# Kernel tuning notes

Hardware: AMD Instinct MI355X
Metric: run time of the kernel (lower is better)

Reference implementation:

```python
import jax, jax.numpy as jnp
import numpy as np

NUM_HEADS = 12
FEATURE_DIM = 16
HEAD_DIM = 128
EPS = 1e-12


def taylor_map(x):
    # x: [b, h, t, d] -> [b, h, t, 1 + d + d*d] (2nd-order Taylor features of exp)
    d = x.shape[-1]
    r2 = jnp.asarray(np.sqrt(2.0), x.dtype)
    rd = jnp.asarray(np.sqrt(d), x.dtype)
    rrd = jnp.asarray(np.sqrt(np.sqrt(d)), x.dtype)
    x2 = (x[..., :, None] * x[..., None, :]).reshape(x.shape[:-1] + (d * d,)) / r2
    ones = jnp.ones(x.shape[:-1] + (1,), x.dtype)
    return jnp.concatenate([ones, x / rrd, x2 / rd], axis=-1)


def setup_inputs() -> dict:
    key = jax.random.key(0)
    ks = jax.random.split(key, 5)
    b, t, hid = 2, 2048, 1536
    scale = 0.02
    return {
        "hidden_states": jax.random.normal(ks[0], (b, t, hid), jnp.float32),
        "Wq": jax.random.normal(ks[1], (NUM_HEADS * FEATURE_DIM, hid), jnp.float32) * scale,
        "Wk": jax.random.normal(ks[2], (NUM_HEADS * FEATURE_DIM, hid), jnp.float32) * scale,
        "Wv": jax.random.normal(ks[3], (NUM_HEADS * HEAD_DIM, hid), jnp.float32) * scale,
        "Wo": jax.random.normal(ks[4], (hid, NUM_HEADS * HEAD_DIM), jnp.float32) * scale,
    }


def reference(hidden_states, Wq, Wk, Wv, Wo):
    b, t, _ = hidden_states.shape
    H, dk, dv = NUM_HEADS, FEATURE_DIM, HEAD_DIM
    # projections (torch Linear: x @ W^T), split heads -> [b, h, t, d]
    q = (hidden_states @ Wq.T).reshape(b, t, H, dk).transpose(0, 2, 1, 3)
    k = (hidden_states @ Wk.T).reshape(b, t, H, dk).transpose(0, 2, 1, 3)
    v = (hidden_states @ Wv.T).reshape(b, t, H, dv).transpose(0, 2, 1, 3)
    qf = taylor_map(q)  # [b, h, t, D], D = 1 + dk + dk^2
    kf = taylor_map(k)
    # causal kernelized attention: identical math to cumsum-of-outer-products form
    S = jnp.einsum("bhtd,bhsd->bhts", qf, kf)  # [b, h, t, t]
    mask = jnp.tril(jnp.ones((t, t), bool))
    S = jnp.where(mask, S, jnp.zeros((), S.dtype))
    num = jnp.einsum("bhts,bhse->bhte", S, v)  # [b, h, t, dv]
    den = S.sum(-1) + EPS  # [b, h, t]
    y = num / den[..., None]
    y = y.transpose(0, 2, 1, 3).reshape(b, t, H * dv)
    return y @ Wo.T
```

## Files before the change

### kernel.cpp

```cpp
#include <hip/hip_runtime.h>

#define B 2
#define T 2048
#define HID 1536
#define NH 12
#define DK 16
#define DV 128
#define BT (B * T)
#define EPS 1e-12f

typedef __attribute__((ext_vector_type(8))) short bf16x8;
typedef __attribute__((ext_vector_type(4))) float f32x4;

__device__ __forceinline__ unsigned short f2bf(float f) {
    unsigned int u = __float_as_uint(f);
    u += 0x7FFFu + ((u >> 16) & 1u);
    return (unsigned short)(u >> 16);
}

__global__ __launch_bounds__(256) void cvt_all(const float* __restrict__ hs,
                                               const float* __restrict__ Wq,
                                               const float* __restrict__ Wk,
                                               const float* __restrict__ Wv,
                                               const float* __restrict__ Wo,
                                               unsigned short* __restrict__ hsb,
                                               unsigned short* __restrict__ wqk,
                                               unsigned short* __restrict__ wvb,
                                               unsigned short* __restrict__ wob) {
    int bx = blockIdx.x;
    const float* src;
    unsigned short* dst;
    if (bx < 3072)      { src = hs; dst = hsb; }
    else if (bx < 3216) { src = Wq; dst = wqk;          bx -= 3072; }
    else if (bx < 3360) { src = Wk; dst = wqk + 294912; bx -= 3216; }
    else if (bx < 4512) { src = Wv; dst = wvb;          bx -= 3360; }
    else                { src = Wo; dst = wob;          bx -= 4512; }
    const int i = (bx * 256 + threadIdx.x) * 8;
    float4 a = *(const float4*)(src + i);
    float4 b = *(const float4*)(src + i + 4);
    *(ushort4*)(dst + i)     = make_ushort4(f2bf(a.x), f2bf(a.y), f2bf(a.z), f2bf(a.w));
    *(ushort4*)(dst + i + 4) = make_ushort4(f2bf(b.x), f2bf(b.y), f2bf(b.z), f2bf(b.w));
}

__device__ __forceinline__ void gemm_tile_bf16(const unsigned short* __restrict__ A,
                                               const unsigned short* __restrict__ Bm,
                                               unsigned short* __restrict__ C,
                                               int m0, int n0, int K, int ldc,
                                               unsigned short* As, unsigned short* Bs) {
    const int tid = threadIdx.x;
    const int wave = tid >> 6, lane = tid & 63;
    const int wm = (wave & 1) * 64, wn = (wave >> 1) * 64;
    const int fr = lane & 15;
    const int fk = (lane >> 4) * 8;

    f32x4 acc[4][4];
#pragma unroll
    for (int i = 0; i < 4; ++i)
#pragma unroll
        for (int j = 0; j < 4; ++j) acc[i][j] = (f32x4)0.f;

    const int c0 = tid, c1 = tid + 256;
    const int r0 = c0 >> 2, q0 = (c0 & 3) * 8;
    const int r1 = c1 >> 2, q1 = (c1 & 3) * 8;

    for (int k0 = 0; k0 < K; k0 += 32) {
        __builtin_amdgcn_global_load_lds(
            (const __attribute__((address_space(1))) void*)(A + (size_t)(m0 + r0) * K + k0 + q0),
            (__attribute__((address_space(3))) void*)(As + c0 * 8), 16, 0, 0);
        __builtin_amdgcn_global_load_lds(
            (const __attribute__((address_space(1))) void*)(A + (size_t)(m0 + r1) * K + k0 + q1),
            (__attribute__((address_space(3))) void*)(As + c1 * 8), 16, 0, 0);
        __builtin_amdgcn_global_load_lds(
            (const __attribute__((address_space(1))) void*)(Bm + (size_t)(n0 + r0) * K + k0 + q0),
            (__attribute__((address_space(3))) void*)(Bs + c0 * 8), 16, 0, 0);
        __builtin_amdgcn_global_load_lds(
            (const __attribute__((address_space(1))) void*)(Bm + (size_t)(n0 + r1) * K + k0 + q1),
            (__attribute__((address_space(3))) void*)(Bs + c1 * 8), 16, 0, 0);
        __syncthreads();

        bf16x8 af[4], bfr[4];
#pragma unroll
        for (int mb = 0; mb < 4; ++mb)
            af[mb] = *(const bf16x8*)(As + (wm + mb * 16 + fr) * 32 + fk);
#pragma unroll
        for (int nb = 0; nb < 4; ++nb)
            bfr[nb] = *(const bf16x8*)(Bs + (wn + nb * 16 + fr) * 32 + fk);
#pragma unroll
        for (int mb = 0; mb < 4; ++mb)
#pragma unroll
            for (int nb = 0; nb < 4; ++nb)
                acc[mb][nb] = __builtin_amdgcn_mfma_f32_16x16x32_bf16(
                    af[mb], bfr[nb], acc[mb][nb], 0, 0, 0);
        __syncthreads();
    }

    const int orow = (lane >> 4) * 4;
#pragma unroll
    for (int nb = 0; nb < 4; ++nb) {
        const int col = n0 + wn + nb * 16 + fr;
#pragma unroll
        for (int mb = 0; mb < 4; ++mb) {
            const int row = m0 + wm + mb * 16 + orow;
#pragma unroll
            for (int r = 0; r < 4; ++r)
                C[(size_t)(row + r) * ldc + col] = f2bf(acc[mb][nb][r]);
        }
    }
}

__global__ __launch_bounds__(256) void proj_qkv(const unsigned short* __restrict__ hsb,
                                                const unsigned short* __restrict__ wqk,
                                                const unsigned short* __restrict__ wvb,
                                                unsigned short* __restrict__ qkb,
                                                unsigned short* __restrict__ vtg) {
    __shared__ unsigned short As[128 * 32];
    __shared__ unsigned short Bs[128 * 32];
    const int bx = blockIdx.x;
    if (bx < 96) {
        gemm_tile_bf16(hsb, wqk, qkb, (bx / 3) * 128, (bx % 3) * 128, HID, 384, As, Bs);
    } else {
        const int vid = bx - 96;
        const int grp = vid / 48, sub = vid % 48;
        const int n_t = grp * 4 + (sub & 3), m_t = sub >> 2;
        gemm_tile_bf16(wvb, hsb, vtg, m_t * 128, n_t * 128, HID, BT, As, Bs);
    }
}

__global__ __launch_bounds__(256) void proj_out(const unsigned short* __restrict__ A,
                                                const unsigned short* __restrict__ Bm,
                                                float* __restrict__ C) {
    __shared__ unsigned short As[128 * 32];
    __shared__ unsigned short Bs[128 * 32];
    const int tid = threadIdx.x;
    const int m0 = blockIdx.y * 128;
    const int n0 = blockIdx.x * 128;
    const int wave = tid >> 6, lane = tid & 63;
    const int wm = (wave & 1) * 64, wn = (wave >> 1) * 64;
    const int fr = lane & 15;
    const int fk = (lane >> 4) * 8;
    const int K = HID;

    f32x4 acc[4][4];
#pragma unroll
    for (int i = 0; i < 4; ++i)
#pragma unroll
        for (int j = 0; j < 4; ++j) acc[i][j] = (f32x4)0.f;

    const int c0 = tid, c1 = tid + 256;
    const int r0 = c0 >> 2, q0 = (c0 & 3) * 8;
    const int r1 = c1 >> 2, q1 = (c1 & 3) * 8;

    for (int k0 = 0; k0 < K; k0 += 32) {
        __builtin_amdgcn_global_load_lds(
            (const __attribute__((address_space(1))) void*)(A + (size_t)(m0 + r0) * K + k0 + q0),
            (__attribute__((address_space(3))) void*)(As + c0 * 8), 16, 0, 0);
        __builtin_amdgcn_global_load_lds(
            (const __attribute__((address_space(1))) void*)(A + (size_t)(m0 + r1) * K + k0 + q1),
            (__attribute__((address_space(3))) void*)(As + c1 * 8), 16, 0, 0);
        __builtin_amdgcn_global_load_lds(
            (const __attribute__((address_space(1))) void*)(Bm + (size_t)(n0 + r0) * K + k0 + q0),
            (__attribute__((address_space(3))) void*)(Bs + c0 * 8), 16, 0, 0);
        __builtin_amdgcn_global_load_lds(
            (const __attribute__((address_space(1))) void*)(Bm + (size_t)(n0 + r1) * K + k0 + q1),
            (__attribute__((address_space(3))) void*)(Bs + c1 * 8), 16, 0, 0);
        __syncthreads();

        bf16x8 af[4], bfr[4];
#pragma unroll
        for (int mb = 0; mb < 4; ++mb)
            af[mb] = *(const bf16x8*)(As + (wm + mb * 16 + fr) * 32 + fk);
#pragma unroll
        for (int nb = 0; nb < 4; ++nb)
            bfr[nb] = *(const bf16x8*)(Bs + (wn + nb * 16 + fr) * 32 + fk);
#pragma unroll
        for (int mb = 0; mb < 4; ++mb)
#pragma unroll
            for (int nb = 0; nb < 4; ++nb)
                acc[mb][nb] = __builtin_amdgcn_mfma_f32_16x16x32_bf16(
                    af[mb], bfr[nb], acc[mb][nb], 0, 0, 0);
        __syncthreads();
    }

    const int orow = (lane >> 4) * 4;
#pragma unroll
    for (int nb = 0; nb < 4; ++nb) {
        const int col = n0 + wn + nb * 16 + fr;
#pragma unroll
        for (int mb = 0; mb < 4; ++mb) {
            const int row = m0 + wm + mb * 16 + orow;
#pragma unroll
            for (int r = 0; r < 4; ++r)
                C[(size_t)(row + r) * HID + col] = acc[mb][nb][r];
        }
    }
}

__global__ __launch_bounds__(256) void based_attn_mfma(const unsigned short* __restrict__ qk,
                                                       const unsigned short* __restrict__ vt,
                                                       unsigned short* __restrict__ yb) {
    const int bx = blockIdx.x;
    const int qt = (T / 64 - 1) - (bx / (NH * B));
    const int hb = bx % (NH * B);
    const int h  = hb >> 1;
    const int bi = hb & 1;
    const int tid = threadIdx.x;
    const int wave = tid >> 6, lane = tid & 63;
    const int fr = lane & 15, quad = lane >> 4;
    const int fk = quad * 8;
    const int fkk = (quad & 1) * 8;

    __shared__ __attribute__((aligned(16))) unsigned short ss[2][64][72];
    __shared__ float den_lds[64];
    if (tid < 64) den_lds[tid] = 0.f;

    const bf16x8 zf = {};
    bf16x8 qf[4];
#pragma unroll
    for (int nt = 0; nt < 4; ++nt) {
        qf[nt] = zf;
        if (quad < 2)
            qf[nt] = *(const bf16x8*)&qk[(size_t)(bi * T + qt * 64 + nt * 16 + fr) * 384
                                         + h * DK + fk];
    }

    f32x4 oacc[2][4];
#pragma unroll
    for (int mt = 0; mt < 2; ++mt)
#pragma unroll
        for (int nt = 0; nt < 4; ++nt) oacc[mt][nt] = (f32x4)0.f;
    float denp[4] = {0.f, 0.f, 0.f, 0.f};

    const unsigned short* kbase = qk + (size_t)(bi * T + wave * 16 + fr) * 384 + 192 + h * DK + fkk;
    const unsigned short* vbase0 = vt + (size_t)(h * DV + wave * 32 + fr) * BT + bi * T + fk;
    const unsigned short* vbase1 = vbase0 + (size_t)16 * BT;

    bf16x8 kf_n = *(const bf16x8*)kbase;
    bf16x8 vf_n[2][2];
    vf_n[0][0] = *(const bf16x8*)(vbase0);
    vf_n[0][1] = *(const bf16x8*)(vbase0 + 32);
    vf_n[1][0] = *(const bf16x8*)(vbase1);
    vf_n[1][1] = *(const bf16x8*)(vbase1 + 32);

    for (int kt = 0; kt <= qt; ++kt) {
        const int bsel = kt & 1;
        const bf16x8 kf = kf_n;
        bf16x8 vf[2][2];
        vf[0][0] = vf_n[0][0]; vf[0][1] = vf_n[0][1];
        vf[1][0] = vf_n[1][0]; vf[1][1] = vf_n[1][1];

        {
            const int ktn = (kt < qt) ? kt + 1 : qt;
            kf_n = *(const bf16x8*)(kbase + (size_t)ktn * 64 * 384);
            const int off = ktn * 64;
            vf_n[0][0] = *(const bf16x8*)(vbase0 + off);
            vf_n[0][1] = *(const bf16x8*)(vbase0 + off + 32);
            vf_n[1][0] = *(const bf16x8*)(vbase1 + off);
            vf_n[1][1] = *(const bf16x8*)(vbase1 + off + 32);
        }

        f32x4 sa[4];
#pragma unroll
        for (int nt = 0; nt < 4; ++nt)
            sa[nt] = __builtin_amdgcn_mfma_f32_16x16x32_bf16(kf, qf[nt], (f32x4)0.f, 0, 0, 0);

#pragma unroll
        for (int nt = 0; nt < 4; ++nt) {
            const int i = nt * 16 + fr;
            float sv[4];
#pragma unroll
            for (int r = 0; r < 4; ++r) {
                const float a = sa[nt][r];
                sv[r] = fmaf(a, fmaf(a, 1.f / 32.f, 0.25f), 1.f);
            }
            if (kt == qt) {
#pragma unroll
                for (int r = 0; r < 4; ++r) {
                    const int j = wave * 16 + quad * 4 + r;
                    if (j > i) sv[r] = 0.f;
                }
            }
            denp[nt] += sv[0] + sv[1] + sv[2] + sv[3];
            uint2 pk;
            pk.x = (__float_as_uint(sv[0]) >> 16) | (__float_as_uint(sv[1]) & 0xFFFF0000u);
            pk.y = (__float_as_uint(sv[2]) >> 16) | (__float_as_uint(sv[3]) & 0xFFFF0000u);
            *(uint2*)&ss[bsel][i][wave * 16 + quad * 4] = pk;
        }
        __syncthreads();

#pragma unroll
        for (int k2 = 0; k2 < 2; ++k2) {
            bf16x8 sf[4];
#pragma unroll
            for (int nt = 0; nt < 4; ++nt)
                sf[nt] = *(const bf16x8*)&ss[bsel][nt * 16 + fr][k2 * 32 + fk];
#pragma unroll
            for (int mt = 0; mt < 2; ++mt)
#pragma unroll
                for (int nt = 0; nt < 4; ++nt)
                    oacc[mt][nt] = __builtin_amdgcn_mfma_f32_16x16x32_bf16(
                        vf[mt][k2], sf[nt], oacc[mt][nt], 0, 0, 0);
        }
    }

#pragma unroll
    for (int nt = 0; nt < 4; ++nt) {
        float v = denp[nt];
        v += __shfl_xor(v, 16);
        v += __shfl_xor(v, 32);
        if (quad == 0) atomicAdd(&den_lds[nt * 16 + fr], v);
    }
    __syncthreads();

#pragma unroll
    for (int nt = 0; nt < 4; ++nt) {
        const int i = nt * 16 + fr;
        const float rd = 1.f / (den_lds[i] + EPS);
        const size_t rowbase = (size_t)(bi * T + qt * 64 + i) * (NH * DV) + h * DV;
#pragma unroll
        for (int mt = 0; mt < 2; ++mt) {
            const int c = wave * 32 + mt * 16 + quad * 4;
            const f32x4 o = oacc[mt][nt];
            *(ushort4*)&yb[rowbase + c] = make_ushort4(f2bf(o[0] * rd), f2bf(o[1] * rd),
                                                       f2bf(o[2] * rd), f2bf(o[3] * rd));
        }
    }
}

extern "C" void kernel_launch(void* const* d_in, const int* in_sizes, int n_in,
                              void* d_out, int out_size, void* d_ws, size_t ws_size,
                              hipStream_t stream) {
    (void)in_sizes; (void)n_in; (void)out_size; (void)ws_size;
    const float* hs = (const float*)d_in[0];
    const float* Wq = (const float*)d_in[1];
    const float* Wk = (const float*)d_in[2];
    const float* Wv = (const float*)d_in[3];
    const float* Wo = (const float*)d_in[4];
    float* out = (float*)d_out;

    unsigned short* hsb = (unsigned short*)d_ws;
    unsigned short* wqk = hsb + (size_t)BT * HID;
    unsigned short* wvb = wqk + (size_t)384 * HID;
    unsigned short* wob = wvb + (size_t)HID * HID;
    unsigned short* qkb = wob + (size_t)HID * HID;
    unsigned short* vtg = qkb + (size_t)BT * 384;
    unsigned short* ybb = vtg + (size_t)HID * BT;

    dim3 blk(256);
    cvt_all<<<dim3(5664), blk, 0, stream>>>(hs, Wq, Wk, Wv, Wo, hsb, wqk, wvb, wob);

    proj_qkv<<<dim3(480), blk, 0, stream>>>(hsb, wqk, wvb, qkb, vtg);

    based_attn_mfma<<<dim3(T / 64 * NH * B), blk, 0, stream>>>(qkb, vtg, ybb);

    proj_out<<<dim3(12, 32), blk, 0, stream>>>(ybb, wob, out);
}
```

Measured before the change: 213.5 us.

## Split causal key range across two wave groups per attention block

```diff
diff --git a/kernel.cpp b/kernel.cpp
--- a/kernel.cpp
+++ b/kernel.cpp
@@ -16,6 +16,12 @@
     unsigned int u = __float_as_uint(f);
     u += 0x7FFFu + ((u >> 16) & 1u);
     return (unsigned short)(u >> 16);
+}
+
+__device__ __forceinline__ unsigned int cvt_pk_bf16(float lo, float hi) {
+    unsigned int r;
+    asm("v_cvt_pk_bf16_f32 %0, %1, %2" : "=v"(r) : "v"(lo), "v"(hi));
+    return r;
 }
 
 __global__ __launch_bounds__(256) void cvt_all(const float* __restrict__ hs,
@@ -195,7 +201,7 @@
     }
 }
 
-__global__ __launch_bounds__(256) void based_attn_mfma(const unsigned short* __restrict__ qk,
+__global__ __launch_bounds__(512) void based_attn_mfma(const unsigned short* __restrict__ qk,
                                                        const unsigned short* __restrict__ vt,
                                                        unsigned short* __restrict__ yb) {
     const int bx = blockIdx.x;
@@ -204,13 +210,21 @@
     const int h  = hb >> 1;
     const int bi = hb & 1;
     const int tid = threadIdx.x;
-    const int wave = tid >> 6, lane = tid & 63;
+    const int wave = tid >> 6;
+    const int g = wave >> 2, w4 = wave & 3;
+    const int lane = tid & 63;
     const int fr = lane & 15, quad = lane >> 4;
     const int fk = quad * 8;
     const int fkk = (quad & 1) * 8;
 
-    __shared__ __attribute__((aligned(16))) unsigned short ss[2][64][72];
+    const int nlow = (qt + 2) >> 1;
+    const int kstart = g ? nlow : 0;
+
+    __shared__ __attribute__((aligned(16))) unsigned short ssmem[2 * 2 * 64 * 72];
     __shared__ float den_lds[64];
+    unsigned short (*ss)[64][72] = (unsigned short (*)[64][72])(ssmem + g * (2 * 64 * 72));
+    float* ob = (float*)ssmem;
+
     if (tid < 64) den_lds[tid] = 0.f;
 
     const bf16x8 zf = {};
@@ -230,19 +244,23 @@
         for (int nt = 0; nt < 4; ++nt) oacc[mt][nt] = (f32x4)0.f;
     float denp[4] = {0.f, 0.f, 0.f, 0.f};
 
-    const unsigned short* kbase = qk + (size_t)(bi * T + wave * 16 + fr) * 384 + 192 + h * DK + fkk;
-    const unsigned short* vbase0 = vt + (size_t)(h * DV + wave * 32 + fr) * BT + bi * T + fk;
+    const unsigned short* kbase = qk + (size_t)(bi * T + w4 * 16 + fr) * 384 + 192 + h * DK + fkk;
+    const unsigned short* vbase0 = vt + (size_t)(h * DV + w4 * 32 + fr) * BT + bi * T + fk;
     const unsigned short* vbase1 = vbase0 + (size_t)16 * BT;
 
-    bf16x8 kf_n = *(const bf16x8*)kbase;
+    bf16x8 kf_n = *(const bf16x8*)(kbase + (size_t)kstart * 64 * 384);
     bf16x8 vf_n[2][2];
-    vf_n[0][0] = *(const bf16x8*)(vbase0);
-    vf_n[0][1] = *(const bf16x8*)(vbase0 + 32);
-    vf_n[1][0] = *(const bf16x8*)(vbase1);
-    vf_n[1][1] = *(const bf16x8*)(vbase1 + 32);
-
-    for (int kt = 0; kt <= qt; ++kt) {
-        const int bsel = kt & 1;
+    {
+        const int off = kstart * 64;
+        vf_n[0][0] = *(const bf16x8*)(vbase0 + off);
+        vf_n[0][1] = *(const bf16x8*)(vbase0 + off + 32);
+        vf_n[1][0] = *(const bf16x8*)(vbase1 + off);
+        vf_n[1][1] = *(const bf16x8*)(vbase1 + off + 32);
+    }
+
+    for (int it = 0; it < nlow; ++it) {
+        const int kt = kstart + it;
+        const int bsel = it & 1;
         const bf16x8 kf = kf_n;
         bf16x8 vf[2][2];
         vf[0][0] = vf_n[0][0]; vf[0][1] = vf_n[0][1];
@@ -272,18 +290,18 @@
                 const float a = sa[nt][r];
                 sv[r] = fmaf(a, fmaf(a, 1.f / 32.f, 0.25f), 1.f);
             }
-            if (kt == qt) {
+            if (kt >= qt) {
 #pragma unroll
                 for (int r = 0; r < 4; ++r) {
-                    const int j = wave * 16 + quad * 4 + r;
-                    if (j > i) sv[r] = 0.f;
+                    const int jg = kt * 64 + w4 * 16 + quad * 4 + r;
+                    if (jg > qt * 64 + i) sv[r] = 0.f;
                 }
             }
-            denp[nt] += sv[0] + sv[1] + sv[2] + sv[3];
+            denp[nt] += (sv[0] + sv[1]) + (sv[2] + sv[3]);
             uint2 pk;
-            pk.x = (__float_as_uint(sv[0]) >> 16) | (__float_as_uint(sv[1]) & 0xFFFF0000u);
-            pk.y = (__float_as_uint(sv[2]) >> 16) | (__float_as_uint(sv[3]) & 0xFFFF0000u);
-            *(uint2*)&ss[bsel][i][wave * 16 + quad * 4] = pk;
+            pk.x = cvt_pk_bf16(sv[0], sv[1]);
+            pk.y = cvt_pk_bf16(sv[2], sv[3]);
+            *(uint2*)&ss[bsel][i][w4 * 16 + quad * 4] = pk;
         }
         __syncthreads();
 
@@ -311,17 +329,37 @@
     }
     __syncthreads();
 
-#pragma unroll
-    for (int nt = 0; nt < 4; ++nt) {
-        const int i = nt * 16 + fr;
-        const float rd = 1.f / (den_lds[i] + EPS);
-        const size_t rowbase = (size_t)(bi * T + qt * 64 + i) * (NH * DV) + h * DV;
-#pragma unroll
-        for (int mt = 0; mt < 2; ++mt) {
-            const int c = wave * 32 + mt * 16 + quad * 4;
-            const f32x4 o = oacc[mt][nt];
-            *(ushort4*)&yb[rowbase + c] = make_ushort4(f2bf(o[0] * rd), f2bf(o[1] * rd),
-                                                       f2bf(o[2] * rd), f2bf(o[3] * rd));
+    if (g == 1) {
+#pragma unroll
+        for (int mt = 0; mt < 2; ++mt)
+#pragma unroll
+            for (int nt = 0; nt < 4; ++nt) {
+                const int c = w4 * 32 + mt * 16 + quad * 4;
+                const int i = nt * 16 + fr;
+#pragma unroll
+                for (int r = 0; r < 4; ++r)
+                    ob[(size_t)(c + r) * 66 + i] = oacc[mt][nt][r];
+            }
+    }
+    __syncthreads();
+
+    if (g == 0) {
+#pragma unroll
+        for (int nt = 0; nt < 4; ++nt) {
+            const int i = nt * 16 + fr;
+            const float rd = 1.f / (den_lds[i] + EPS);
+            const size_t rowbase = (size_t)(bi * T + qt * 64 + i) * (NH * DV) + h * DV;
+#pragma unroll
+            for (int mt = 0; mt < 2; ++mt) {
+                const int c = w4 * 32 + mt * 16 + quad * 4;
+                const f32x4 o = oacc[mt][nt];
+                float o0 = o[0] + ob[(size_t)(c + 0) * 66 + i];
+                float o1 = o[1] + ob[(size_t)(c + 1) * 66 + i];
+                float o2 = o[2] + ob[(size_t)(c + 2) * 66 + i];
+                float o3 = o[3] + ob[(size_t)(c + 3) * 66 + i];
+                *(ushort4*)&yb[rowbase + c] = make_ushort4(f2bf(o0 * rd), f2bf(o1 * rd),
+                                                           f2bf(o2 * rd), f2bf(o3 * rd));
+            }
         }
     }
 }
@@ -350,7 +388,7 @@
 
     proj_qkv<<<dim3(480), blk, 0, stream>>>(hsb, wqk, wvb, qkb, vtg);
 
-    based_attn_mfma<<<dim3(T / 64 * NH * B), blk, 0, stream>>>(qkb, vtg, ybb);
+    based_attn_mfma<<<dim3(T / 64 * NH * B), dim3(512), 0, stream>>>(qkb, vtg, ybb);
 
     proj_out<<<dim3(12, 32), blk, 0, stream>>>(ybb, wob, out);
 }
```

After: 213.6 us. Within noise of the previous version (+0.0%).

## Make causal attention kernel persistent with atomic work queue and paired tile ordering

Applied to the files above, without the earlier changes.

```diff
diff --git a/kernel.cpp b/kernel.cpp
--- a/kernel.cpp
+++ b/kernel.cpp
@@ -12,10 +12,18 @@
 typedef __attribute__((ext_vector_type(8))) short bf16x8;
 typedef __attribute__((ext_vector_type(4))) float f32x4;
 
+__device__ int g_taskctr;
+
 __device__ __forceinline__ unsigned short f2bf(float f) {
     unsigned int u = __float_as_uint(f);
     u += 0x7FFFu + ((u >> 16) & 1u);
     return (unsigned short)(u >> 16);
+}
+
+__device__ __forceinline__ unsigned int cvt_pk_bf16(float lo, float hi) {
+    unsigned int r;
+    asm("v_cvt_pk_bf16_f32 %0, %1, %2" : "=v"(r) : "v"(lo), "v"(hi));
+    return r;
 }
 
 __global__ __launch_bounds__(256) void cvt_all(const float* __restrict__ hs,
@@ -28,6 +36,7 @@
                                                unsigned short* __restrict__ wvb,
                                                unsigned short* __restrict__ wob) {
     int bx = blockIdx.x;
+    if (bx == 0 && threadIdx.x == 0) g_taskctr = 512;
     const float* src;
     unsigned short* dst;
     if (bx < 3072)      { src = hs; dst = hsb; }
@@ -198,11 +207,6 @@
 __global__ __launch_bounds__(256) void based_attn_mfma(const unsigned short* __restrict__ qk,
                                                        const unsigned short* __restrict__ vt,
                                                        unsigned short* __restrict__ yb) {
-    const int bx = blockIdx.x;
-    const int qt = (T / 64 - 1) - (bx / (NH * B));
-    const int hb = bx % (NH * B);
-    const int h  = hb >> 1;
-    const int bi = hb & 1;
     const int tid = threadIdx.x;
     const int wave = tid >> 6, lane = tid & 63;
     const int fr = lane & 15, quad = lane >> 4;
@@ -211,118 +215,137 @@
 
     __shared__ __attribute__((aligned(16))) unsigned short ss[2][64][72];
     __shared__ float den_lds[64];
-    if (tid < 64) den_lds[tid] = 0.f;
-
-    const bf16x8 zf = {};
-    bf16x8 qf[4];
-#pragma unroll
-    for (int nt = 0; nt < 4; ++nt) {
-        qf[nt] = zf;
-        if (quad < 2)
-            qf[nt] = *(const bf16x8*)&qk[(size_t)(bi * T + qt * 64 + nt * 16 + fr) * 384
-                                         + h * DK + fk];
-    }
-
-    f32x4 oacc[2][4];
-#pragma unroll
-    for (int mt = 0; mt < 2; ++mt)
-#pragma unroll
-        for (int nt = 0; nt < 4; ++nt) oacc[mt][nt] = (f32x4)0.f;
-    float denp[4] = {0.f, 0.f, 0.f, 0.f};
-
-    const unsigned short* kbase = qk + (size_t)(bi * T + wave * 16 + fr) * 384 + 192 + h * DK + fkk;
-    const unsigned short* vbase0 = vt + (size_t)(h * DV + wave * 32 + fr) * BT + bi * T + fk;
-    const unsigned short* vbase1 = vbase0 + (size_t)16 * BT;
-
-    bf16x8 kf_n = *(const bf16x8*)kbase;
-    bf16x8 vf_n[2][2];
-    vf_n[0][0] = *(const bf16x8*)(vbase0);
-    vf_n[0][1] = *(const bf16x8*)(vbase0 + 32);
-    vf_n[1][0] = *(const bf16x8*)(vbase1);
-    vf_n[1][1] = *(const bf16x8*)(vbase1 + 32);
-
-    for (int kt = 0; kt <= qt; ++kt) {
-        const int bsel = kt & 1;
-        const bf16x8 kf = kf_n;
-        bf16x8 vf[2][2];
-        vf[0][0] = vf_n[0][0]; vf[0][1] = vf_n[0][1];
-        vf[1][0] = vf_n[1][0]; vf[1][1] = vf_n[1][1];
-
-        {
-            const int ktn = (kt < qt) ? kt + 1 : qt;
-            kf_n = *(const bf16x8*)(kbase + (size_t)ktn * 64 * 384);
-            const int off = ktn * 64;
-            vf_n[0][0] = *(const bf16x8*)(vbase0 + off);
-            vf_n[0][1] = *(const bf16x8*)(vbase0 + off + 32);
-            vf_n[1][0] = *(const bf16x8*)(vbase1 + off);
-            vf_n[1][1] = *(const bf16x8*)(vbase1 + off + 32);
-        }
-
-        f32x4 sa[4];
-#pragma unroll
-        for (int nt = 0; nt < 4; ++nt)
-            sa[nt] = __builtin_amdgcn_mfma_f32_16x16x32_bf16(kf, qf[nt], (f32x4)0.f, 0, 0, 0);
+    __shared__ int task_s;
+
+    int c = blockIdx.x;
+
+    for (;;) {
+        if (c >= 768) break;
+        const int r = (c < 512) ? ((c & 1) ? 767 - (c >> 1) : (c >> 1)) : (c - 256);
+        const int qt = 31 - r / 24;
+        const int hb = r % 24;
+        const int h  = hb >> 1;
+        const int bi = hb & 1;
+
+        if (tid < 64) den_lds[tid] = 0.f;
+
+        const bf16x8 zf = {};
+        bf16x8 qf[4];
+#pragma unroll
+        for (int nt = 0; nt < 4; ++nt) {
+            qf[nt] = zf;
+            if (quad < 2)
+                qf[nt] = *(const bf16x8*)&qk[(size_t)(bi * T + qt * 64 + nt * 16 + fr) * 384
+                                             + h * DK + fk];
+        }
+
+        f32x4 oacc[2][4];
+#pragma unroll
+        for (int mt = 0; mt < 2; ++mt)
+#pragma unroll
+            for (int nt = 0; nt < 4; ++nt) oacc[mt][nt] = (f32x4)0.f;
+        float denp[4] = {0.f, 0.f, 0.f, 0.f};
+
+        const unsigned short* kbase = qk + (size_t)(bi * T + wave * 16 + fr) * 384
+                                      + 192 + h * DK + fkk;
+        const unsigned short* vbase0 = vt + (size_t)(h * DV + wave * 32 + fr) * BT + bi * T + fk;
+        const unsigned short* vbase1 = vbase0 + (size_t)16 * BT;
+
+        bf16x8 kf_n = *(const bf16x8*)kbase;
+        bf16x8 vf_n[2][2];
+        vf_n[0][0] = *(const bf16x8*)(vbase0);
+        vf_n[0][1] = *(const bf16x8*)(vbase0 + 32);
+        vf_n[1][0] = *(const bf16x8*)(vbase1);
+        vf_n[1][1] = *(const bf16x8*)(vbase1 + 32);
+
+        for (int kt = 0; kt <= qt; ++kt) {
+            const int bsel = kt & 1;
+            const bf16x8 kf = kf_n;
+            bf16x8 vf[2][2];
+            vf[0][0] = vf_n[0][0]; vf[0][1] = vf_n[0][1];
+            vf[1][0] = vf_n[1][0]; vf[1][1] = vf_n[1][1];
+
+            {
+                const int ktn = (kt < qt) ? kt + 1 : qt;
+                kf_n = *(const bf16x8*)(kbase + (size_t)ktn * 64 * 384);
+                const int off = ktn * 64;
+                vf_n[0][0] = *(const bf16x8*)(vbase0 + off);
+                vf_n[0][1] = *(const bf16x8*)(vbase0 + off + 32);
+                vf_n[1][0] = *(const bf16x8*)(vbase1 + off);
+                vf_n[1][1] = *(const bf16x8*)(vbase1 + off + 32);
+            }
+
+            f32x4 sa[4];
+#pragma unroll
+            for (int nt = 0; nt < 4; ++nt)
+                sa[nt] = __builtin_amdgcn_mfma_f32_16x16x32_bf16(kf, qf[nt], (f32x4)0.f, 0, 0, 0);
+
+#pragma unroll
+            for (int nt = 0; nt < 4; ++nt) {
+                const int i = nt * 16 + fr;
+                float sv[4];
+#pragma unroll
+                for (int rr = 0; rr < 4; ++rr) {
+                    const float a = sa[nt][rr];
+                    sv[rr] = fmaf(a, fmaf(a, 1.f / 32.f, 0.25f), 1.f);
+                }
+                if (kt == qt) {
+#pragma unroll
+                    for (int rr = 0; rr < 4; ++rr) {
+                        const int j = wave * 16 + quad * 4 + rr;
+                        if (j > i) sv[rr] = 0.f;
+                    }
+                }
+                denp[nt] += (sv[0] + sv[1]) + (sv[2] + sv[3]);
+                uint2 pk;
+                pk.x = cvt_pk_bf16(sv[0], sv[1]);
+                pk.y = cvt_pk_bf16(sv[2], sv[3]);
+                *(uint2*)&ss[bsel][i][wave * 16 + quad * 4] = pk;
+            }
+            __syncthreads();
+
+#pragma unroll
+            for (int k2 = 0; k2 < 2; ++k2) {
+                bf16x8 sf[4];
+#pragma unroll
+                for (int nt = 0; nt < 4; ++nt)
+                    sf[nt] = *(const bf16x8*)&ss[bsel][nt * 16 + fr][k2 * 32 + fk];
+#pragma unroll
+                for (int mt = 0; mt < 2; ++mt)
+#pragma unroll
+                    for (int nt = 0; nt < 4; ++nt)
+                        oacc[mt][nt] = __builtin_amdgcn_mfma_f32_16x16x32_bf16(
+                            vf[mt][k2], sf[nt], oacc[mt][nt], 0, 0, 0);
+            }
+        }
+
+#pragma unroll
+        for (int nt = 0; nt < 4; ++nt) {
+            float v = denp[nt];
+            v += __shfl_xor(v, 16);
+            v += __shfl_xor(v, 32);
+            if (quad == 0) atomicAdd(&den_lds[nt * 16 + fr], v);
+        }
+        __syncthreads();
 
 #pragma unroll
         for (int nt = 0; nt < 4; ++nt) {
             const int i = nt * 16 + fr;
-            float sv[4];
-#pragma unroll
-            for (int r = 0; r < 4; ++r) {
-                const float a = sa[nt][r];
-                sv[r] = fmaf(a, fmaf(a, 1.f / 32.f, 0.25f), 1.f);
+            const float rd = 1.f / (den_lds[i] + EPS);
+            const size_t rowbase = (size_t)(bi * T + qt * 64 + i) * (NH * DV) + h * DV;
+#pragma unroll
+            for (int mt = 0; mt < 2; ++mt) {
+                const int cc = wave * 32 + mt * 16 + quad * 4;
+                const f32x4 o = oacc[mt][nt];
+                *(ushort4*)&yb[rowbase + cc] = make_ushort4(f2bf(o[0] * rd), f2bf(o[1] * rd),
+                                                            f2bf(o[2] * rd), f2bf(o[3] * rd));
             }
-            if (kt == qt) {
-#pragma unroll
-                for (int r = 0; r < 4; ++r) {
-                    const int j = wave * 16 + quad * 4 + r;
-                    if (j > i) sv[r] = 0.f;
-                }
-            }
-            denp[nt] += sv[0] + sv[1] + sv[2] + sv[3];
-            uint2 pk;
-            pk.x = (__float_as_uint(sv[0]) >> 16) | (__float_as_uint(sv[1]) & 0xFFFF0000u);
-            pk.y = (__float_as_uint(sv[2]) >> 16) | (__float_as_uint(sv[3]) & 0xFFFF0000u);
-            *(uint2*)&ss[bsel][i][wave * 16 + quad * 4] = pk;
-        }
-        __syncthreads();
-
-#pragma unroll
-        for (int k2 = 0; k2 < 2; ++k2) {
-            bf16x8 sf[4];
-#pragma unroll
-            for (int nt = 0; nt < 4; ++nt)
-                sf[nt] = *(const bf16x8*)&ss[bsel][nt * 16 + fr][k2 * 32 + fk];
-#pragma unroll
-            for (int mt = 0; mt < 2; ++mt)
-#pragma unroll
-                for (int nt = 0; nt < 4; ++nt)
-                    oacc[mt][nt] = __builtin_amdgcn_mfma_f32_16x16x32_bf16(
-                        vf[mt][k2], sf[nt], oacc[mt][nt], 0, 0, 0);
-        }
-    }
-
-#pragma unroll
-    for (int nt = 0; nt < 4; ++nt) {
-        float v = denp[nt];
-        v += __shfl_xor(v, 16);
-        v += __shfl_xor(v, 32);
-        if (quad == 0) atomicAdd(&den_lds[nt * 16 + fr], v);
-    }
-    __syncthreads();
-
-#pragma unroll
-    for (int nt = 0; nt < 4; ++nt) {
-        const int i = nt * 16 + fr;
-        const float rd = 1.f / (den_lds[i] + EPS);
-        const size_t rowbase = (size_t)(bi * T + qt * 64 + i) * (NH * DV) + h * DV;
-#pragma unroll
-        for (int mt = 0; mt < 2; ++mt) {
-            const int c = wave * 32 + mt * 16 + quad * 4;
-            const f32x4 o = oacc[mt][nt];
-            *(ushort4*)&yb[rowbase + c] = make_ushort4(f2bf(o[0] * rd), f2bf(o[1] * rd),
-                                                       f2bf(o[2] * rd), f2bf(o[3] * rd));
-        }
+        }
+
+        __syncthreads();
+        if (tid == 0) task_s = atomicAdd(&g_taskctr, 1);
+        __syncthreads();
+        c = task_s;
     }
 }
 
@@ -350,7 +373,7 @@
 
     proj_qkv<<<dim3(480), blk, 0, stream>>>(hsb, wqk, wvb, qkb, vtg);
 
-    based_attn_mfma<<<dim3(T / 64 * NH * B), blk, 0, stream>>>(qkb, vtg, ybb);
+    based_attn_mfma<<<dim3(512), blk, 0, stream>>>(qkb, vtg, ybb);
 
     proj_out<<<dim3(12, 32), blk, 0, stream>>>(ybb, wob, out);
 }
```

Result: no change. 209.7 us (-1.8%).
